# Kernel tuning notes

Measured on AMD Instinct MI355X. Metric: run time of the kernel, lower is better.

## Reference

```python
import jax, jax.numpy as jnp
import numpy as np

DIM = 128
WIN = (2, 7, 7)
HEADS = 4
N = WIN[0] * WIN[1] * WIN[2]  # 98
B_ = 2048
NW = 256  # num windows per sample; B_ // NW = batch = 8


def _relative_position_index(win):
    t = np.arange(win[0]); h = np.arange(win[1]); w = np.arange(win[2])
    coords = np.stack(np.meshgrid(t, h, w, indexing='ij'))  # (3, T, H, W)
    cf = coords.reshape(3, -1)  # (3, N)
    rel = cf[:, :, None] - cf[:, None, :]  # (3, N, N)
    rel = rel.transpose(1, 2, 0).copy()
    rel[:, :, 0] += win[0] - 1
    rel[:, :, 1] += win[1] - 1
    rel[:, :, 2] += win[2] - 1
    rel[:, :, 0] *= (2 * win[1] - 1) * (2 * win[2] - 1)
    rel[:, :, 1] *= 2 * win[2] - 1
    return rel.sum(-1).astype(np.int32)  # (N, N)


def setup_inputs() -> dict:
    key = jax.random.key(0)
    ks = jax.random.split(key, 8)
    table_len = (2 * WIN[0] - 1) * (2 * WIN[1] - 1) * (2 * WIN[2] - 1)  # 507
    x = jax.random.normal(ks[0], (B_, N, DIM), dtype=jnp.float32)
    # 0 / -inf style additive mask (use -1e4 as finite -inf)
    u = jax.random.uniform(ks[1], (NW, N, N))
    mask = jnp.where(u < 0.9, 0.0, -1e4).astype(jnp.float32)
    qkv_w = jax.random.normal(ks[2], (3 * DIM, DIM), dtype=jnp.float32) * (DIM ** -0.5)
    qkv_b = jax.random.normal(ks[3], (3 * DIM,), dtype=jnp.float32) * 0.02
    proj_w = jax.random.normal(ks[4], (DIM, DIM), dtype=jnp.float32) * (DIM ** -0.5)
    proj_b = jax.random.normal(ks[5], (DIM,), dtype=jnp.float32) * 0.02
    bias_table = jax.random.normal(ks[6], (table_len, HEADS), dtype=jnp.float32) * 0.02
    rel_index = jnp.asarray(_relative_position_index(WIN))
    return {"x": x, "mask": mask, "qkv_w": qkv_w, "qkv_b": qkv_b,
            "proj_w": proj_w, "proj_b": proj_b, "bias_table": bias_table,
            "rel_index": rel_index}


def reference(x, mask, qkv_w, qkv_b, proj_w, proj_b, bias_table, rel_index):
    Bq, n, c = x.shape
    hd = c // HEADS
    scale = hd ** -0.5
    qkv = x @ qkv_w.T + qkv_b  # (B_, N, 3C)
    qkv = qkv.reshape(Bq, n, 3, HEADS, hd).transpose(2, 0, 3, 1, 4)  # (3, B_, H, N, hd)
    q, k, v = qkv[0] * scale, qkv[1], qkv[2]
    attn = jnp.einsum('bhnd,bhmd->bhnm', q, k)  # (B_, H, N, N)
    bias = bias_table[rel_index.reshape(-1)].reshape(n, n, HEADS)
    attn = attn + bias.transpose(2, 0, 1)[None]  # add (1, H, N, N)
    nW = mask.shape[0]
    attn = attn.reshape(Bq // nW, nW, HEADS, n, n) + mask[None, :, None]
    attn = jax.nn.softmax(attn.reshape(Bq, HEADS, n, n), axis=-1)
    out = jnp.einsum('bhnm,bhmd->bhnd', attn, v)  # (B_, H, N, hd)
    out = out.transpose(0, 2, 1, 3).reshape(Bq, n, c)
    return out @ proj_w.T + proj_b
```

## Files before the change

### kernel.cpp

```cpp
#include <hip/hip_runtime.h>
#include <hip/hip_bf16.h>


#define NTOK 98
#define NN (NTOK * NTOK)
#define SCALE 0.17677669529663687f

typedef short bf16x8 __attribute__((ext_vector_type(8)));
typedef float f32x4 __attribute__((ext_vector_type(4)));
#define MFMA(a, b, c) __builtin_amdgcn_mfma_f32_16x16x32_bf16(a, b, c, 0, 0, 0)

static __device__ __forceinline__ unsigned short f2bf(float f) {
  union { float f; unsigned int i; } x; x.f = f;
  unsigned int u = x.i;
  unsigned int rnd = ((u >> 16) & 1u) + 0x7fffu;
  return (unsigned short)((u + rnd) >> 16);
}
static __device__ __forceinline__ float bf2f(short s) {
  union { unsigned int i; float f; } x;
  x.i = ((unsigned int)(unsigned short)s) << 16;
  return x.f;
}

__global__ void k0_w(const float* __restrict__ qkv_w, const float* __restrict__ proj_w,
                     unsigned short* __restrict__ wqb, unsigned short* __restrict__ wpb) {
  int idx = blockIdx.x * 256 + threadIdx.x;
  if (idx < 49152) wqb[idx] = f2bf(qkv_w[idx]);
  else wpb[idx - 49152] = f2bf(proj_w[idx - 49152]);
}

__global__ void k0b_bm(const float* __restrict__ table, const int* __restrict__ rel,
                       const float* __restrict__ mask, unsigned short* __restrict__ bm) {
  const int wmodh = blockIdx.x, mt = blockIdx.y;
  const int wmod = wmodh >> 2, h = wmodh & 3;
  const int t = threadIdx.x;
  const int lane = t >> 2, reg = t & 3;
  const int quad = lane >> 4, L15 = lane & 15;
  const int row = mt * 16 + quad * 4 + reg;
  bf16x8 v8;
#pragma unroll
  for (int nt = 0; nt < 8; ++nt) {
    float v = -1.0e30f;
    int col = nt * 16 + L15;
    if (nt < 7 && row < NTOK && col < NTOK) {
      int nm = row * NTOK + col;
      v = table[rel[nm] * 4 + h] + mask[(size_t)wmod * NN + nm];
    }
    v8[nt] = (short)f2bf(v);
  }
  *(bf16x8*)&bm[(((size_t)wmodh * 7 + mt) << 11) + (lane << 5) + (reg << 3)] = v8;
}

__global__ __launch_bounds__(256) void k1_qkv(const float* __restrict__ x,
                                              const unsigned short* __restrict__ wqb,
                                              const float* __restrict__ qkv_b,
                                              unsigned short* __restrict__ q,
                                              unsigned short* __restrict__ k,
                                              unsigned short* __restrict__ v) {
  __shared__ unsigned short xt[64 * 136];
  __shared__ unsigned short wt[128 * 136];
  const int t = threadIdx.x;
  const int r0 = blockIdx.x * 64;
  const int wv = t >> 6, lane = t & 63, L15 = lane & 15, quad = lane >> 4;

#pragma unroll
  for (int i = 0; i < 8; ++i) {
    int idx = t + (i << 8);
    int row = idx >> 5, c4 = idx & 31;
    float4 xv = *(const float4*)&x[(size_t)(r0 + row) * 128 + c4 * 4];
    ushort4 pk; pk.x = f2bf(xv.x); pk.y = f2bf(xv.y); pk.z = f2bf(xv.z); pk.w = f2bf(xv.w);
    *(ushort4*)&xt[row * 136 + c4 * 4] = pk;
  }

  bf16x8 af[4];
  bool afLoaded = false;

  for (int g = 0; g < 3; ++g) {
    if (g) __syncthreads();
#pragma unroll
    for (int i = 0; i < 8; ++i) {
      int idx = t + (i << 8);
      int c = idx >> 4, kq = idx & 15;
      *(uint4*)&wt[c * 136 + kq * 8] = ((const uint4*)wqb)[g * 2048 + idx];
    }
    __syncthreads();
    if (!afLoaded) {
      afLoaded = true;
#pragma unroll
      for (int kt = 0; kt < 4; ++kt)
        af[kt] = *(const bf16x8*)&xt[(wv * 16 + L15) * 136 + kt * 32 + quad * 8];
    }

    f32x4 acc[8];
#pragma unroll
    for (int nt = 0; nt < 8; ++nt) {
      f32x4 a = {0.f, 0.f, 0.f, 0.f};
#pragma unroll
      for (int kt = 0; kt < 4; ++kt) {
        bf16x8 bf_ = *(const bf16x8*)&wt[(nt * 16 + L15) * 136 + kt * 32 + quad * 8];
        a = MFMA(af[kt], bf_, a);
      }
      acc[nt] = a;
    }

    unsigned short* dst = (g == 0) ? q : ((g == 1) ? k : v);
    const float sc = (g == 0) ? SCALE : 1.0f;
    float bias[8];
#pragma unroll
    for (int nt = 0; nt < 8; ++nt) bias[nt] = qkv_b[g * 128 + nt * 16 + L15];
#pragma unroll
    for (int reg = 0; reg < 4; ++reg) {
      int R = r0 + wv * 16 + quad * 4 + reg;
      int b = R / NTOK, n = R - b * NTOK;
      size_t base0 = ((size_t)b * 4 * NTOK + n) * 32;
#pragma unroll
      for (int nt = 0; nt < 8; ++nt) {
        int h = nt >> 1, dd = ((nt & 1) << 4) + L15;
        float val = (acc[nt][reg] + bias[nt]) * sc;
        dst[base0 + (size_t)h * (NTOK * 32) + dd] = f2bf(val);
      }
    }
  }
}

__global__ __launch_bounds__(256) void k2_attn(const unsigned short* __restrict__ qg,
                                               const unsigned short* __restrict__ kg,
                                               const unsigned short* __restrict__ vg,
                                               const unsigned short* __restrict__ bm,
                                               unsigned short* __restrict__ og) {
  __shared__ unsigned short sK[112 * 40];
  __shared__ unsigned short sVt[32 * 136];
  __shared__ unsigned short sP[4 * 16 * 136];
  const int t = threadIdx.x;
  const int bh = blockIdx.x, bw = bh >> 2, h = bh & 3;
  const int wmodh = ((bw & 255) << 2) + h;
  const size_t base = (size_t)bh * (NTOK * 32);
  const int wv = t >> 6, lane = t & 63, L15 = lane & 15, quad = lane >> 4;
  unsigned short* myP = sP + wv * (16 * 136);

  for (int i = t; i < 2240; i += 256) ((unsigned int*)sK)[i] = 0;
  for (int j = lane; j < 128; j += 64) {
    int r = j >> 3, cp = j & 7;
    *(unsigned int*)&myP[r * 136 + 112 + cp * 2] = 0;
  }
  __syncthreads();
  for (int i = t; i < 392; i += 256) {
    int row = i >> 2, kq = i & 3;
    *(uint4*)&sK[row * 40 + kq * 8] = ((const uint4*)kg)[(size_t)bh * 392 + i];
  }
  for (int i = t; i < 3136; i += 256) {
    int n = i >> 5, d = i & 31;
    sVt[d * 136 + n] = vg[base + i];
  }
  __syncthreads();

  auto strip = [&](int mt) {
    const unsigned short* bmp = bm + (((size_t)wmodh * 7 + mt) << 11) + (lane << 5);
    bf16x8 bmv[4];
#pragma unroll
    for (int reg = 0; reg < 4; ++reg) bmv[reg] = *(const bf16x8*)&bmp[reg << 3];
    bf16x8 aq = *(const bf16x8*)&qg[base + (size_t)(mt * 16 + L15) * 32 + quad * 8];
    f32x4 s[7];
#pragma unroll
    for (int nt = 0; nt < 7; ++nt) {
      bf16x8 bk = *(const bf16x8*)&sK[(nt * 16 + L15) * 40 + quad * 8];
      f32x4 z = {0.f, 0.f, 0.f, 0.f};
      s[nt] = MFMA(aq, bk, z);
    }
#pragma unroll
    for (int reg = 0; reg < 4; ++reg) {
      float mx = -3.0e38f;
#pragma unroll
      for (int nt = 0; nt < 7; ++nt) {
        float val = s[nt][reg] + bf2f(bmv[reg][nt]);
        s[nt][reg] = val;
        mx = fmaxf(mx, val);
      }
#pragma unroll
      for (int d = 1; d < 16; d <<= 1) mx = fmaxf(mx, __shfl_xor(mx, d, 64));
      float sum = 0.f;
#pragma unroll
      for (int nt = 0; nt < 7; ++nt) {
        float e = __expf(s[nt][reg] - mx);
        s[nt][reg] = e; sum += e;
      }
#pragma unroll
      for (int d = 1; d < 16; d <<= 1) sum += __shfl_xor(sum, d, 64);
      float rs = 1.0f / sum;
#pragma unroll
      for (int nt = 0; nt < 7; ++nt)
        myP[(quad * 4 + reg) * 136 + nt * 16 + L15] = f2bf(s[nt][reg] * rs);
    }
    f32x4 o0 = {0.f, 0.f, 0.f, 0.f}, o1 = {0.f, 0.f, 0.f, 0.f};
#pragma unroll
    for (int kt = 0; kt < 4; ++kt) {
      bf16x8 ap  = *(const bf16x8*)&myP[L15 * 136 + kt * 32 + quad * 8];
      bf16x8 bv0 = *(const bf16x8*)&sVt[L15 * 136 + kt * 32 + quad * 8];
      bf16x8 bv1 = *(const bf16x8*)&sVt[(16 + L15) * 136 + kt * 32 + quad * 8];
      o0 = MFMA(ap, bv0, o0);
      o1 = MFMA(ap, bv1, o1);
    }
#pragma unroll
    for (int reg = 0; reg < 4; ++reg) {
      int n = mt * 16 + quad * 4 + reg;
      if (n < NTOK) {
        size_t ob = ((size_t)bw * NTOK + n) * 128 + h * 32;
        og[ob + L15]      = f2bf(o0[reg]);
        og[ob + 16 + L15] = f2bf(o1[reg]);
      }
    }
  };
  strip(wv * 2);
  if (wv < 3) strip(wv * 2 + 1);
}

__global__ __launch_bounds__(256) void k3_proj(const unsigned short* __restrict__ og,
                                               const unsigned short* __restrict__ wpb,
                                               const float* __restrict__ pb,
                                               float* __restrict__ out) {
  __shared__ unsigned short ot[64 * 136];
  __shared__ unsigned short wt[128 * 136];
  const int t = threadIdx.x;
  const int r0 = blockIdx.x * 64;
  const int wv = t >> 6, lane = t & 63, L15 = lane & 15, quad = lane >> 4;

#pragma unroll
  for (int i = 0; i < 4; ++i) {
    int idx = t + (i << 8);
    int row = idx >> 4, kq = idx & 15;
    *(uint4*)&ot[row * 136 + kq * 8] = ((const uint4*)og)[(size_t)(r0 + row) * 16 + kq];
  }
#pragma unroll
  for (int i = 0; i < 8; ++i) {
    int idx = t + (i << 8);
    int c = idx >> 4, kq = idx & 15;
    *(uint4*)&wt[c * 136 + kq * 8] = ((const uint4*)wpb)[idx];
  }
  __syncthreads();

  bf16x8 af[4];
#pragma unroll
  for (int kt = 0; kt < 4; ++kt)
    af[kt] = *(const bf16x8*)&ot[(wv * 16 + L15) * 136 + kt * 32 + quad * 8];

  f32x4 acc[8];
#pragma unroll
  for (int nt = 0; nt < 8; ++nt) {
    f32x4 a = {0.f, 0.f, 0.f, 0.f};
#pragma unroll
    for (int kt = 0; kt < 4; ++kt) {
      bf16x8 bf_ = *(const bf16x8*)&wt[(nt * 16 + L15) * 136 + kt * 32 + quad * 8];
      a = MFMA(af[kt], bf_, a);
    }
    acc[nt] = a;
  }

  float bias[8];
#pragma unroll
  for (int nt = 0; nt < 8; ++nt) bias[nt] = pb[nt * 16 + L15];
#pragma unroll
  for (int reg = 0; reg < 4; ++reg) {
    size_t R = (size_t)(r0 + wv * 16 + quad * 4 + reg);
#pragma unroll
    for (int nt = 0; nt < 8; ++nt)
      out[R * 128 + nt * 16 + L15] = acc[nt][reg] + bias[nt];
  }
}

extern "C" void kernel_launch(void* const* d_in, const int* in_sizes, int n_in,
                              void* d_out, int out_size, void* d_ws, size_t ws_size,
                              hipStream_t stream) {
  (void)in_sizes; (void)n_in; (void)out_size; (void)ws_size;
  const float* x      = (const float*)d_in[0];
  const float* mask   = (const float*)d_in[1];
  const float* qkv_w  = (const float*)d_in[2];
  const float* qkv_b  = (const float*)d_in[3];
  const float* proj_w = (const float*)d_in[4];
  const float* proj_b = (const float*)d_in[5];
  const float* table  = (const float*)d_in[6];
  const int*   rel    = (const int*)d_in[7];
  float* out = (float*)d_out;

  const size_t QS = (size_t)2048 * 4 * NTOK * 32;
  unsigned short* q   = (unsigned short*)d_ws;
  unsigned short* k   = q + QS;
  unsigned short* v   = k + QS;
  unsigned short* o   = v + QS;
  unsigned short* wqb = o + QS;
  unsigned short* wpb = wqb + 49152;
  unsigned short* bm  = (unsigned short*)d_out;

  k0_w<<<256, 256, 0, stream>>>(qkv_w, proj_w, wqb, wpb);
  k0b_bm<<<dim3(1024, 7), 256, 0, stream>>>(table, rel, mask, bm);
  k1_qkv<<<200704 / 64, 256, 0, stream>>>(x, wqb, qkv_b, q, k, v);
  k2_attn<<<2048 * 4, 256, 0, stream>>>(q, k, v, bm, o);
  k3_proj<<<200704 / 64, 256, 0, stream>>>(o, wpb, proj_b, out);
}
```

Before: 378.4 us.

## Preswizzle weights for direct MFMA loads, larger GEMM tiles, max-free exp2 softmax

Weights are stored in MFMA fragment order so the QKV and projection GEMMs read B operands directly from global memory instead of staging them through LDS, and each block now processes 128 rows. The attention softmax folds log2e into the Q scale and bias/mask and drops the max-reduction, using exp2 with a clamp and a fast reciprocal. The V transpose load is vectorised and redundant zero-fill and a barrier are removed. Skipping max subtraction risks overflow or precision loss if scores were large.

```diff
diff --git a/kernel.cpp b/kernel.cpp
--- a/kernel.cpp
+++ b/kernel.cpp
@@ -4,7 +4,8 @@
 
 #define NTOK 98
 #define NN (NTOK * NTOK)
-#define SCALE 0.17677669529663687f
+#define LOG2E 1.4426950408889634f
+#define QSCALE (0.17677669529663687f * LOG2E)
 
 typedef short bf16x8 __attribute__((ext_vector_type(8)));
 typedef float f32x4 __attribute__((ext_vector_type(4)));
@@ -23,10 +24,19 @@
 }
 
 __global__ void k0_w(const float* __restrict__ qkv_w, const float* __restrict__ proj_w,
-                     unsigned short* __restrict__ wqb, unsigned short* __restrict__ wpb) {
+                     unsigned short* __restrict__ wqbf, unsigned short* __restrict__ wpbf) {
   int idx = blockIdx.x * 256 + threadIdx.x;
-  if (idx < 49152) wqb[idx] = f2bf(qkv_w[idx]);
-  else wpb[idx - 49152] = f2bf(proj_w[idx - 49152]);
+  if (idx < 49152) {
+    int j = idx & 7, lane = (idx >> 3) & 63, kt = (idx >> 9) & 3;
+    int nt = (idx >> 11) & 7, g = idx >> 14;
+    int n = nt * 16 + (lane & 15), k = kt * 32 + (lane >> 4) * 8 + j;
+    wqbf[idx] = f2bf(qkv_w[(size_t)(g * 128 + n) * 128 + k]);
+  } else {
+    int i2 = idx - 49152;
+    int j = i2 & 7, lane = (i2 >> 3) & 63, kt = (i2 >> 9) & 3, nt = i2 >> 11;
+    int n = nt * 16 + (lane & 15), k = kt * 32 + (lane >> 4) * 8 + j;
+    wpbf[i2] = f2bf(proj_w[(size_t)n * 128 + k]);
+  }
 }
 
 __global__ void k0b_bm(const float* __restrict__ table, const int* __restrict__ rel,
@@ -44,7 +54,7 @@
     int col = nt * 16 + L15;
     if (nt < 7 && row < NTOK && col < NTOK) {
       int nm = row * NTOK + col;
-      v = table[rel[nm] * 4 + h] + mask[(size_t)wmod * NN + nm];
+      v = (table[rel[nm] * 4 + h] + mask[(size_t)wmod * NN + nm]) * LOG2E;
     }
     v8[nt] = (short)f2bf(v);
   }
@@ -52,72 +62,55 @@
 }
 
 __global__ __launch_bounds__(256) void k1_qkv(const float* __restrict__ x,
-                                              const unsigned short* __restrict__ wqb,
+                                              const unsigned short* __restrict__ wqbf,
                                               const float* __restrict__ qkv_b,
                                               unsigned short* __restrict__ q,
                                               unsigned short* __restrict__ k,
                                               unsigned short* __restrict__ v) {
-  __shared__ unsigned short xt[64 * 136];
-  __shared__ unsigned short wt[128 * 136];
-  const int t = threadIdx.x;
-  const int r0 = blockIdx.x * 64;
+  __shared__ unsigned short xt[128 * 136];
+  const int t = threadIdx.x;
+  const int r0 = blockIdx.x * 128;
   const int wv = t >> 6, lane = t & 63, L15 = lane & 15, quad = lane >> 4;
 
 #pragma unroll
-  for (int i = 0; i < 8; ++i) {
+  for (int i = 0; i < 16; ++i) {
     int idx = t + (i << 8);
     int row = idx >> 5, c4 = idx & 31;
     float4 xv = *(const float4*)&x[(size_t)(r0 + row) * 128 + c4 * 4];
     ushort4 pk; pk.x = f2bf(xv.x); pk.y = f2bf(xv.y); pk.z = f2bf(xv.z); pk.w = f2bf(xv.w);
     *(ushort4*)&xt[row * 136 + c4 * 4] = pk;
   }
-
-  bf16x8 af[4];
-  bool afLoaded = false;
+  __syncthreads();
+
+  bf16x8 af[2][4];
+#pragma unroll
+  for (int p = 0; p < 2; ++p)
+#pragma unroll
+    for (int kt = 0; kt < 4; ++kt)
+      af[p][kt] = *(const bf16x8*)&xt[(wv * 32 + p * 16 + L15) * 136 + kt * 32 + quad * 8];
 
   for (int g = 0; g < 3; ++g) {
-    if (g) __syncthreads();
-#pragma unroll
-    for (int i = 0; i < 8; ++i) {
-      int idx = t + (i << 8);
-      int c = idx >> 4, kq = idx & 15;
-      *(uint4*)&wt[c * 136 + kq * 8] = ((const uint4*)wqb)[g * 2048 + idx];
-    }
-    __syncthreads();
-    if (!afLoaded) {
-      afLoaded = true;
-#pragma unroll
-      for (int kt = 0; kt < 4; ++kt)
-        af[kt] = *(const bf16x8*)&xt[(wv * 16 + L15) * 136 + kt * 32 + quad * 8];
-    }
-
-    f32x4 acc[8];
+    unsigned short* dst = (g == 0) ? q : ((g == 1) ? k : v);
+    const float sc = (g == 0) ? QSCALE : 1.0f;
 #pragma unroll
     for (int nt = 0; nt < 8; ++nt) {
-      f32x4 a = {0.f, 0.f, 0.f, 0.f};
+      f32x4 a0 = {0.f, 0.f, 0.f, 0.f}, a1 = {0.f, 0.f, 0.f, 0.f};
 #pragma unroll
       for (int kt = 0; kt < 4; ++kt) {
-        bf16x8 bf_ = *(const bf16x8*)&wt[(nt * 16 + L15) * 136 + kt * 32 + quad * 8];
-        a = MFMA(af[kt], bf_, a);
-      }
-      acc[nt] = a;
-    }
-
-    unsigned short* dst = (g == 0) ? q : ((g == 1) ? k : v);
-    const float sc = (g == 0) ? SCALE : 1.0f;
-    float bias[8];
-#pragma unroll
-    for (int nt = 0; nt < 8; ++nt) bias[nt] = qkv_b[g * 128 + nt * 16 + L15];
-#pragma unroll
-    for (int reg = 0; reg < 4; ++reg) {
-      int R = r0 + wv * 16 + quad * 4 + reg;
-      int b = R / NTOK, n = R - b * NTOK;
-      size_t base0 = ((size_t)b * 4 * NTOK + n) * 32;
-#pragma unroll
-      for (int nt = 0; nt < 8; ++nt) {
-        int h = nt >> 1, dd = ((nt & 1) << 4) + L15;
-        float val = (acc[nt][reg] + bias[nt]) * sc;
-        dst[base0 + (size_t)h * (NTOK * 32) + dd] = f2bf(val);
+        bf16x8 b = *(const bf16x8*)&wqbf[((((g * 8 + nt) * 4 + kt)) << 9) + lane * 8];
+        a0 = MFMA(af[0][kt], b, a0);
+        a1 = MFMA(af[1][kt], b, a1);
+      }
+      float bias = qkv_b[g * 128 + nt * 16 + L15];
+      int h = nt >> 1, dd = ((nt & 1) << 4) + L15;
+#pragma unroll
+      for (int reg = 0; reg < 4; ++reg) {
+        int R0 = r0 + wv * 32 + quad * 4 + reg;
+        int b0 = R0 / NTOK, n0 = R0 - b0 * NTOK;
+        dst[((size_t)(b0 * 4 + h) * NTOK + n0) * 32 + dd] = f2bf((a0[reg] + bias) * sc);
+        int R1 = R0 + 16;
+        int b1 = R1 / NTOK, n1 = R1 - b1 * NTOK;
+        dst[((size_t)(b1 * 4 + h) * NTOK + n1) * 32 + dd] = f2bf((a1[reg] + bias) * sc);
       }
     }
   }
@@ -134,27 +127,34 @@
   const int t = threadIdx.x;
   const int bh = blockIdx.x, bw = bh >> 2, h = bh & 3;
   const int wmodh = ((bw & 255) << 2) + h;
-  const size_t base = (size_t)bh * (NTOK * 32);
+  const size_t base = (size_t)bh * 3136;
   const int wv = t >> 6, lane = t & 63, L15 = lane & 15, quad = lane >> 4;
   unsigned short* myP = sP + wv * (16 * 136);
 
-  for (int i = t; i < 2240; i += 256) ((unsigned int*)sK)[i] = 0;
+  for (int i = t; i < 280; i += 256) *(unsigned int*)&sK[3920 + i * 2] = 0;
   for (int j = lane; j < 128; j += 64) {
     int r = j >> 3, cp = j & 7;
     *(unsigned int*)&myP[r * 136 + 112 + cp * 2] = 0;
   }
-  __syncthreads();
   for (int i = t; i < 392; i += 256) {
     int row = i >> 2, kq = i & 3;
     *(uint4*)&sK[row * 40 + kq * 8] = ((const uint4*)kg)[(size_t)bh * 392 + i];
   }
-  for (int i = t; i < 3136; i += 256) {
-    int n = i >> 5, d = i & 31;
-    sVt[d * 136 + n] = vg[base + i];
+  for (int i = t; i < 1024; i += 256) {
+    int n = i >> 3, d4 = i & 7;
+    unsigned int ux = 0, uy = 0;
+    if (n < NTOK) {
+      uint2 u = *(const uint2*)&vg[base + n * 32 + d4 * 4];
+      ux = u.x; uy = u.y;
+    }
+    sVt[(d4 * 4 + 0) * 136 + n] = (unsigned short)(ux & 0xffffu);
+    sVt[(d4 * 4 + 1) * 136 + n] = (unsigned short)(ux >> 16);
+    sVt[(d4 * 4 + 2) * 136 + n] = (unsigned short)(uy & 0xffffu);
+    sVt[(d4 * 4 + 3) * 136 + n] = (unsigned short)(uy >> 16);
   }
   __syncthreads();
 
-  auto strip = [&](int mt) {
+  auto do_strip = [&](int mt) {
     const unsigned short* bmp = bm + (((size_t)wmodh * 7 + mt) << 11) + (lane << 5);
     bf16x8 bmv[4];
 #pragma unroll
@@ -169,24 +169,15 @@
     }
 #pragma unroll
     for (int reg = 0; reg < 4; ++reg) {
-      float mx = -3.0e38f;
+      float sum = 0.f;
 #pragma unroll
       for (int nt = 0; nt < 7; ++nt) {
-        float val = s[nt][reg] + bf2f(bmv[reg][nt]);
-        s[nt][reg] = val;
-        mx = fmaxf(mx, val);
-      }
-#pragma unroll
-      for (int d = 1; d < 16; d <<= 1) mx = fmaxf(mx, __shfl_xor(mx, d, 64));
-      float sum = 0.f;
-#pragma unroll
-      for (int nt = 0; nt < 7; ++nt) {
-        float e = __expf(s[nt][reg] - mx);
+        float e = exp2f(fminf(s[nt][reg] + bf2f(bmv[reg][nt]), 80.f));
         s[nt][reg] = e; sum += e;
       }
 #pragma unroll
       for (int d = 1; d < 16; d <<= 1) sum += __shfl_xor(sum, d, 64);
-      float rs = 1.0f / sum;
+      float rs = __builtin_amdgcn_rcpf(sum);
 #pragma unroll
       for (int nt = 0; nt < 7; ++nt)
         myP[(quad * 4 + reg) * 136 + nt * 16 + L15] = f2bf(s[nt][reg] * rs);
@@ -210,60 +201,50 @@
       }
     }
   };
-  strip(wv * 2);
-  if (wv < 3) strip(wv * 2 + 1);
+  do_strip(wv * 2);
+  if (wv < 3) do_strip(wv * 2 + 1);
 }
 
 __global__ __launch_bounds__(256) void k3_proj(const unsigned short* __restrict__ og,
-                                               const unsigned short* __restrict__ wpb,
+                                               const unsigned short* __restrict__ wpbf,
                                                const float* __restrict__ pb,
                                                float* __restrict__ out) {
-  __shared__ unsigned short ot[64 * 136];
-  __shared__ unsigned short wt[128 * 136];
-  const int t = threadIdx.x;
-  const int r0 = blockIdx.x * 64;
+  __shared__ unsigned short ot[128 * 136];
+  const int t = threadIdx.x;
+  const int r0 = blockIdx.x * 128;
   const int wv = t >> 6, lane = t & 63, L15 = lane & 15, quad = lane >> 4;
 
 #pragma unroll
-  for (int i = 0; i < 4; ++i) {
+  for (int i = 0; i < 8; ++i) {
     int idx = t + (i << 8);
     int row = idx >> 4, kq = idx & 15;
     *(uint4*)&ot[row * 136 + kq * 8] = ((const uint4*)og)[(size_t)(r0 + row) * 16 + kq];
   }
-#pragma unroll
-  for (int i = 0; i < 8; ++i) {
-    int idx = t + (i << 8);
-    int c = idx >> 4, kq = idx & 15;
-    *(uint4*)&wt[c * 136 + kq * 8] = ((const uint4*)wpb)[idx];
-  }
   __syncthreads();
 
-  bf16x8 af[4];
-#pragma unroll
-  for (int kt = 0; kt < 4; ++kt)
-    af[kt] = *(const bf16x8*)&ot[(wv * 16 + L15) * 136 + kt * 32 + quad * 8];
-
-  f32x4 acc[8];
+  bf16x8 af[2][4];
+#pragma unroll
+  for (int p = 0; p < 2; ++p)
+#pragma unroll
+    for (int kt = 0; kt < 4; ++kt)
+      af[p][kt] = *(const bf16x8*)&ot[(wv * 32 + p * 16 + L15) * 136 + kt * 32 + quad * 8];
+
 #pragma unroll
   for (int nt = 0; nt < 8; ++nt) {
-    f32x4 a = {0.f, 0.f, 0.f, 0.f};
+    f32x4 a0 = {0.f, 0.f, 0.f, 0.f}, a1 = {0.f, 0.f, 0.f, 0.f};
 #pragma unroll
     for (int kt = 0; kt < 4; ++kt) {
-      bf16x8 bf_ = *(const bf16x8*)&wt[(nt * 16 + L15) * 136 + kt * 32 + quad * 8];
-      a = MFMA(af[kt], bf_, a);
-    }
-    acc[nt] = a;
-  }
-
-  float bias[8];
-#pragma unroll
-  for (int nt = 0; nt < 8; ++nt) bias[nt] = pb[nt * 16 + L15];
-#pragma unroll
-  for (int reg = 0; reg < 4; ++reg) {
-    size_t R = (size_t)(r0 + wv * 16 + quad * 4 + reg);
-#pragma unroll
-    for (int nt = 0; nt < 8; ++nt)
-      out[R * 128 + nt * 16 + L15] = acc[nt][reg] + bias[nt];
+      bf16x8 b = *(const bf16x8*)&wpbf[((nt * 4 + kt) << 9) + lane * 8];
+      a0 = MFMA(af[0][kt], b, a0);
+      a1 = MFMA(af[1][kt], b, a1);
+    }
+    float bias = pb[nt * 16 + L15];
+#pragma unroll
+    for (int reg = 0; reg < 4; ++reg) {
+      size_t R0 = (size_t)r0 + wv * 32 + quad * 4 + reg;
+      out[R0 * 128 + nt * 16 + L15] = a0[reg] + bias;
+      out[(R0 + 16) * 128 + nt * 16 + L15] = a1[reg] + bias;
+    }
   }
 }
 
@@ -282,17 +263,17 @@
   float* out = (float*)d_out;
 
   const size_t QS = (size_t)2048 * 4 * NTOK * 32;
-  unsigned short* q   = (unsigned short*)d_ws;
-  unsigned short* k   = q + QS;
-  unsigned short* v   = k + QS;
-  unsigned short* o   = v + QS;
-  unsigned short* wqb = o + QS;
-  unsigned short* wpb = wqb + 49152;
-  unsigned short* bm  = (unsigned short*)d_out;
-
-  k0_w<<<256, 256, 0, stream>>>(qkv_w, proj_w, wqb, wpb);
+  unsigned short* q    = (unsigned short*)d_ws;
+  unsigned short* k    = q + QS;
+  unsigned short* v    = k + QS;
+  unsigned short* o    = v + QS;
+  unsigned short* wqbf = o + QS;
+  unsigned short* wpbf = wqbf + 49152;
+  unsigned short* bm   = (unsigned short*)d_out;
+
+  k0_w<<<256, 256, 0, stream>>>(qkv_w, proj_w, wqbf, wpbf);
   k0b_bm<<<dim3(1024, 7), 256, 0, stream>>>(table, rel, mask, bm);
-  k1_qkv<<<200704 / 64, 256, 0, stream>>>(x, wqb, qkv_b, q, k, v);
+  k1_qkv<<<200704 / 128, 256, 0, stream>>>(x, wqbf, qkv_b, q, k, v);
   k2_attn<<<2048 * 4, 256, 0, stream>>>(q, k, v, bm, o);
-  k3_proj<<<200704 / 64, 256, 0, stream>>>(o, wpb, proj_b, out);
-}
+  k3_proj<<<200704 / 128, 256, 0, stream>>>(o, wpbf, proj_b, out);
+}
```

New measurement: 428.1 us. +13.1%, slower.
